# Optimization experiments

Measured on AMD Instinct MI355X. Metric: run time of the kernel, lower is better.

Reference implementation:

```python
import jax, jax.numpy as jnp
import numpy as np

# dims: B batch, R seq_num (MSA rows), L seq_len (residues), D emb_dim, C n_emb_2D, H heads
B, R, L, D, C, H = 1, 256, 384, 512, 256, 4
HD = D // H
SCALE = np.float32((HD ** -0.5) / np.sqrt(L))  # head-dim scaling * seqlen_scaling (1/sqrt(L))
EPS = 1e-5


def setup_inputs() -> dict:
    key = jax.random.key(0)
    ks = jax.random.split(key, 6)
    s = 0.02
    return {
        "x": jax.random.normal(ks[0], (B, R, L, D), jnp.float32),
        "pair_feat": jax.random.normal(ks[1], (B, L, L, C), jnp.float32),
        "attn_mask": jnp.ones((B, L), jnp.int32),
        "ln_msa_g": jnp.ones((D,), jnp.float32),
        "ln_msa_b": jnp.zeros((D,), jnp.float32),
        "ln_pair_g": jnp.ones((C,), jnp.float32),
        "ln_pair_b": jnp.zeros((C,), jnp.float32),
        "W_pair": jax.random.normal(ks[2], (C, H), jnp.float32) * s,  # stacked per-head [C,1] linears
        "W_v": jax.random.normal(ks[3], (D, D), jnp.float32) * s,     # stacked per-head [D,HD] value proj
        "W_out": jax.random.normal(ks[4], (D, D), jnp.float32) * s,   # to_out (bias=False)
    }


def _ln(x, g, b):
    mu = jnp.mean(x, axis=-1, keepdims=True)
    var = jnp.mean(jnp.square(x - mu), axis=-1, keepdims=True)
    return (x - mu) * jax.lax.rsqrt(var + EPS) * g + b


def reference(x, pair_feat, attn_mask, ln_msa_g, ln_msa_b, ln_pair_g, ln_pair_b, W_pair, W_v, W_out):
    # MHPair_to_MSA.forward (eval mode, dropout=0)
    msa = _ln(x, ln_msa_g, ln_msa_b)                                  # [B,R,L,D]
    pf = (pair_feat + jnp.swapaxes(pair_feat, 1, 2)) * 0.5            # symmetrize
    pf = _ln(pf, ln_pair_g, ln_pair_b)                                # [B,L,L,C]
    # pair-feature-derived attention logits (no QK^T)
    logits = jnp.einsum('bijc,ch->bhij', pf * SCALE, W_pair)          # [B,H,L,L]
    V = jnp.einsum('brld,de->brle', msa, W_v).reshape(B, R, L, H, HD) # [B,R,L,H,HD]
    mask2 = attn_mask[:, :, None] * attn_mask[:, None, :]             # [B,L,L]
    logits = jnp.where(mask2[:, None, :, :] == 0,
                       jnp.finfo(logits.dtype).min, logits)
    attn = jax.nn.softmax(logits, axis=-1)                            # [B,H,L,L]
    out = jnp.einsum('bhij,brjhd->brihd', attn, V).reshape(B, R, L, D)
    out = out @ W_out                                                 # to_out, bias=False
    return x + out                                                    # residual
```

## Files before the change

### kernel.cpp

```cpp
#include <hip/hip_runtime.h>

#define L_   384
#define D_   512
#define C_   256
#define H_   4
#define RR_  256
#define M1_  98304
#define LL2_ 147456
#define NPAIR_BLOCKS 18480

typedef __bf16 bf16x8 __attribute__((ext_vector_type(8)));
typedef float f32x4 __attribute__((ext_vector_type(4)));

__device__ __forceinline__ unsigned short f2bf_bits(float f) {
  union { float f; unsigned u; } v; v.f = f;
  return (unsigned short)((v.u + 0x7fffu + ((v.u >> 16) & 1u)) >> 16);
}
__device__ __forceinline__ __bf16 f2bf(float f) {
  union { unsigned short s; __bf16 b; } o; o.s = f2bf_bits(f);
  return o.b;
}

__global__ __launch_bounds__(256) void ln_msa_kernel(
    const float* __restrict__ x, const float* __restrict__ g,
    const float* __restrict__ b, __bf16* __restrict__ msa) {
  int row = blockIdx.x * 4 + (threadIdx.x >> 6);
  int lane = threadIdx.x & 63;
  const float4* xr = (const float4*)(x + (size_t)row * D_ + lane * 8);
  float4 v0 = xr[0], v1 = xr[1];
  float s1 = v0.x + v0.y + v0.z + v0.w + v1.x + v1.y + v1.z + v1.w;
  float s2 = v0.x * v0.x + v0.y * v0.y + v0.z * v0.z + v0.w * v0.w +
             v1.x * v1.x + v1.y * v1.y + v1.z * v1.z + v1.w * v1.w;
#pragma unroll
  for (int o = 32; o > 0; o >>= 1) {
    s1 += __shfl_xor(s1, o);
    s2 += __shfl_xor(s2, o);
  }
  float mu = s1 * (1.0f / D_);
  float var = s2 * (1.0f / D_) - mu * mu;
  float rs = rsqrtf(var + 1e-5f);
  const float4* gp = (const float4*)(g + lane * 8);
  const float4* bp = (const float4*)(b + lane * 8);
  float4 g0 = gp[0], g1 = gp[1], b0 = bp[0], b1 = bp[1];
  float y[8];
  y[0] = (v0.x - mu) * rs * g0.x + b0.x;
  y[1] = (v0.y - mu) * rs * g0.y + b0.y;
  y[2] = (v0.z - mu) * rs * g0.z + b0.z;
  y[3] = (v0.w - mu) * rs * g0.w + b0.w;
  y[4] = (v1.x - mu) * rs * g1.x + b1.x;
  y[5] = (v1.y - mu) * rs * g1.y + b1.y;
  y[6] = (v1.z - mu) * rs * g1.z + b1.z;
  y[7] = (v1.w - mu) * rs * g1.w + b1.w;
  uint4 pk;
  pk.x = ((unsigned)f2bf_bits(y[1]) << 16) | f2bf_bits(y[0]);
  pk.y = ((unsigned)f2bf_bits(y[3]) << 16) | f2bf_bits(y[2]);
  pk.z = ((unsigned)f2bf_bits(y[5]) << 16) | f2bf_bits(y[4]);
  pk.w = ((unsigned)f2bf_bits(y[7]) << 16) | f2bf_bits(y[6]);
  *(uint4*)(msa + (size_t)row * D_ + lane * 8) = pk;
}

__global__ __launch_bounds__(256) void pair_logits_kernel(
    const float* __restrict__ pf, const int* __restrict__ mask,
    const float* __restrict__ g, const float* __restrict__ b,
    const float* __restrict__ Wp, float* __restrict__ logits) {
  unsigned wid = blockIdx.x * 4 + (threadIdx.x >> 6);
  int lane = threadIdx.x & 63;
  unsigned a = wid / 385u;
  unsigned c = wid - a * 385u;
  int i, j;
  if (c < 384u - a) { i = a; j = a + c; }
  else { i = 383 - a; j = i + (c - (384 - a)); }

  int c0 = lane * 4;
  float4 p1 = *(const float4*)(pf + ((size_t)i * L_ + j) * C_ + c0);
  float4 p2 = *(const float4*)(pf + ((size_t)j * L_ + i) * C_ + c0);
  float4 v;
  v.x = 0.5f * (p1.x + p2.x); v.y = 0.5f * (p1.y + p2.y);
  v.z = 0.5f * (p1.z + p2.z); v.w = 0.5f * (p1.w + p2.w);
  float s1 = v.x + v.y + v.z + v.w;
  float s2 = v.x * v.x + v.y * v.y + v.z * v.z + v.w * v.w;
#pragma unroll
  for (int o = 32; o > 0; o >>= 1) {
    s1 += __shfl_xor(s1, o);
    s2 += __shfl_xor(s2, o);
  }
  float mu = s1 * (1.0f / C_);
  float var = s2 * (1.0f / C_) - mu * mu;
  float rs = rsqrtf(var + 1e-5f);
  float4 gv = *(const float4*)(g + c0);
  float4 bv = *(const float4*)(b + c0);
  float y0 = (v.x - mu) * rs * gv.x + bv.x;
  float y1 = (v.y - mu) * rs * gv.y + bv.y;
  float y2 = (v.z - mu) * rs * gv.z + bv.z;
  float y3 = (v.w - mu) * rs * gv.w + bv.w;
  const float4* wp = (const float4*)Wp;
  float4 w0 = wp[c0], w1 = wp[c0 + 1], w2 = wp[c0 + 2], w3 = wp[c0 + 3];
  float4 t;
  t.x = y0 * w0.x + y1 * w1.x + y2 * w2.x + y3 * w3.x;
  t.y = y0 * w0.y + y1 * w1.y + y2 * w2.y + y3 * w3.y;
  t.z = y0 * w0.z + y1 * w1.z + y2 * w2.z + y3 * w3.z;
  t.w = y0 * w0.w + y1 * w1.w + y2 * w2.w + y3 * w3.w;
#pragma unroll
  for (int o = 32; o > 0; o >>= 1) {
    t.x += __shfl_xor(t.x, o);
    t.y += __shfl_xor(t.y, o);
    t.z += __shfl_xor(t.z, o);
    t.w += __shfl_xor(t.w, o);
  }
  if (lane < 8) {
    int h = lane & 3;
    int ii = (lane < 4) ? i : j;
    int jj = (lane < 4) ? j : i;
    bool ok = (mask[i] != 0) && (mask[j] != 0);
    const float NEG = -3.402823466e38f;
    const float SCALE = (float)(0.08838834764831845 / 19.595917942265423);
    float th = (h == 0) ? t.x : (h == 1) ? t.y : (h == 2) ? t.z : t.w;
    logits[(size_t)h * LL2_ + (size_t)ii * L_ + jj] = ok ? SCALE * th : NEG;
  }
}

__global__ __launch_bounds__(256) void softmax_kernel(
    const float* __restrict__ logits, __bf16* __restrict__ attn) {
  int wave = threadIdx.x >> 6, lane = threadIdx.x & 63;
  int row = blockIdx.x * 4 + wave;
  const float* lr = logits + (size_t)row * L_;
  float v[6];
#pragma unroll
  for (int t = 0; t < 6; ++t) v[t] = lr[lane + t * 64];
  float mx = v[0];
#pragma unroll
  for (int t = 1; t < 6; ++t) mx = fmaxf(mx, v[t]);
#pragma unroll
  for (int o = 32; o > 0; o >>= 1) mx = fmaxf(mx, __shfl_xor(mx, o));
  float s = 0.f;
#pragma unroll
  for (int t = 0; t < 6; ++t) { v[t] = __expf(v[t] - mx); s += v[t]; }
#pragma unroll
  for (int o = 32; o > 0; o >>= 1) s += __shfl_xor(s, o);
  float inv = 1.0f / s;
  __bf16* ar = attn + (size_t)row * L_;
#pragma unroll
  for (int t = 0; t < 6; ++t) ar[lane + t * 64] = f2bf(v[t] * inv);
}

__global__ __launch_bounds__(256) void wtrans_kernel(
    const float* __restrict__ Wv, const float* __restrict__ Wo,
    __bf16* __restrict__ WvT, __bf16* __restrict__ WoT) {
  int id = blockIdx.x * 256 + threadIdx.x;
  int m = id >> 18;
  int e = (id >> 9) & 511, d = id & 511;
  const float* W = m ? Wo : Wv;
  __bf16* T = m ? WoT : WvT;
  T[(size_t)e * 512 + d] = f2bf(W[(size_t)d * 512 + e]);
}

__device__ __forceinline__ void gload16(const void* g, void* l) {
  __builtin_amdgcn_global_load_lds(
      (const __attribute__((address_space(1))) void*)g,
      (__attribute__((address_space(3))) void*)l, 16, 0, 0);
}

__device__ __forceinline__ unsigned xcd_swz_768(unsigned bid) {
  return (bid & 7u) * 96u + (bid >> 3);
}

template <int NT>
__device__ __forceinline__ void stage_part32(__bf16* s, const __bf16* g, size_t ld) {
  int tid = threadIdx.x;
#pragma unroll
  for (int i = 0; i < 2; ++i) {
    int cid = i * NT + tid;
    int row = cid >> 2, c = cid & 3;
    int cs = c ^ ((row >> 1) & 3);
    gload16(g + (size_t)row * ld + cs * 8, (char*)s + cid * 16);
  }
}

__device__ __forceinline__ bf16x8 frag_ld32(const __bf16* s, int row, int fk) {
  int c = (fk >> 3) ^ ((row >> 1) & 3);
  return *(const bf16x8*)((const char*)s + row * 64 + c * 16);
}

__device__ __forceinline__ void mainloop256_2s(
    const __bf16* __restrict__ A, size_t ldA,
    const __bf16* __restrict__ B, size_t ldB,
    int K, __bf16* lds, f32x4 acc[8][4]) {
  int lane = threadIdx.x & 63, wave = threadIdx.x >> 6;
  int wm = (wave >> 2) * 128, wn = (wave & 3) * 64;
  int fr = lane & 15, fk = (lane >> 4) * 8;
  int nt = K >> 5;
  const int SLOT = 512 * 32;
  stage_part32<512>(lds, A, ldA);
  stage_part32<512>(lds + 256 * 32, B, ldB);
  for (int t = 0; t < nt; ++t) {
    const __bf16* As = lds + (t & 1) * SLOT;
    const __bf16* Bs = As + 256 * 32;
    if (t + 1 < nt) {
      __bf16* d = lds + ((t + 1) & 1) * SLOT;
      stage_part32<512>(d, A + (size_t)(t + 1) * 32, ldA);
      stage_part32<512>(d + 256 * 32, B + (size_t)(t + 1) * 32, ldB);
      asm volatile("s_waitcnt vmcnt(4)" ::: "memory");
    } else {
      asm volatile("s_waitcnt vmcnt(0)" ::: "memory");
    }
    __builtin_amdgcn_s_barrier();
    bf16x8 bfv[4];
#pragma unroll
    for (int ni = 0; ni < 4; ++ni) bfv[ni] = frag_ld32(Bs, wn + ni * 16 + fr, fk);
#pragma unroll
    for (int half = 0; half < 2; ++half) {
      bf16x8 af[4];
#pragma unroll
      for (int mi = 0; mi < 4; ++mi)
        af[mi] = frag_ld32(As, wm + half * 64 + mi * 16 + fr, fk);
      __builtin_amdgcn_s_setprio(1);
#pragma unroll
      for (int mi = 0; mi < 4; ++mi)
#pragma unroll
        for (int ni = 0; ni < 4; ++ni)
          acc[half * 4 + mi][ni] = __builtin_amdgcn_mfma_f32_16x16x32_bf16(
              af[mi], bfv[ni], acc[half * 4 + mi][ni], 0, 0, 0);
      __builtin_amdgcn_s_setprio(0);
    }
  }
}

__global__ __launch_bounds__(512) void gemm_vt_kernel(
    const __bf16* __restrict__ WvT, const __bf16* __restrict__ msa,
    __bf16* __restrict__ VT) {
  __shared__ __bf16 lds[2 * 512 * 32];
  unsigned swz = xcd_swz_768(blockIdx.x + 2 * blockIdx.y);
  int m0 = (swz & 1) * 256;
  int n0 = (swz >> 1) * 256;
  f32x4 acc[8][4] = {};
  mainloop256_2s(WvT + (size_t)m0 * D_, D_, msa + (size_t)n0 * D_, D_, D_, lds, acc);
  int lane = threadIdx.x & 63, wave = threadIdx.x >> 6;
  int wm = (wave >> 2) * 128, wn = (wave & 3) * 64;
  int cr = (lane >> 4) * 4, cc = lane & 15;
#pragma unroll
  for (int mi = 0; mi < 8; ++mi)
#pragma unroll
    for (int ni = 0; ni < 4; ++ni)
#pragma unroll
      for (int rr = 0; rr < 4; ++rr) {
        int row = m0 + wm + mi * 16 + cr + rr;
        int col = n0 + wn + ni * 16 + cc;
        VT[(size_t)row * M1_ + col] = f2bf(acc[mi][ni][rr]);
      }
}

__global__ __launch_bounds__(512, 1) void attnout_kernel(
    const __bf16* __restrict__ attn, const __bf16* __restrict__ VT,
    const __bf16* __restrict__ WoT, const float* __restrict__ x,
    float* __restrict__ out) {
  __shared__ char lds[98304];
  char* Pl = lds + 65536;
  unsigned swz = xcd_swz_768(blockIdx.x + 3 * blockIdx.y);
  int it = swz % 3u;
  int r  = swz / 3u;
  int tid = threadIdx.x, lane = tid & 63, wave = tid >> 6;
  int fr = lane & 15, fk = (lane >> 4) * 8;
  int cr = (lane >> 4) * 4, cc = lane & 15;
  int wi = (wave >> 2) * 64;
  int we = (wave & 3) * 32;
  int wf = (wave & 3) * 128;

  f32x4 acc_out[4][8] = {};

  for (int h = 0; h < 4; ++h) {
    const __bf16* A = attn + (size_t)h * LL2_ + (size_t)(it * 128) * L_;
    const __bf16* B = VT + (size_t)(h * 128) * M1_ + (size_t)r * L_;

    f32x4 acc_p[4][2] = {};
    {
      const int SLOT = 16384;
      int row = tid >> 2, c = tid & 3;
      int cs = c ^ ((row >> 1) & 3);
      auto stageA = [&](int t) {
        char* d = lds + (t & 3) * SLOT;
        gload16(A + (size_t)row * L_ + t * 32 + cs * 8, d + tid * 16);
        gload16(B + (size_t)row * M1_ + t * 32 + cs * 8, d + 8192 + tid * 16);
      };
      stageA(0); stageA(1); stageA(2);
      for (int t = 0; t < 12; ++t) {
        int rem = 11 - t;
        if (rem >= 2)      asm volatile("s_waitcnt vmcnt(4)" ::: "memory");
        else if (rem == 1) asm volatile("s_waitcnt vmcnt(2)" ::: "memory");
        else               asm volatile("s_waitcnt vmcnt(0)" ::: "memory");
        __builtin_amdgcn_s_barrier();
        const __bf16* As = (const __bf16*)(lds + (t & 3) * SLOT);
        const __bf16* Bs = (const __bf16*)(lds + (t & 3) * SLOT + 8192);
        if (t + 3 < 12) stageA(t + 3);
        bf16x8 af[4], bf2[2];
#pragma unroll
        for (int mi = 0; mi < 4; ++mi) af[mi] = frag_ld32(As, wi + mi * 16 + fr, fk);
#pragma unroll
        for (int ni = 0; ni < 2; ++ni) bf2[ni] = frag_ld32(Bs, we + ni * 16 + fr, fk);
        __builtin_amdgcn_s_setprio(1);
#pragma unroll
        for (int mi = 0; mi < 4; ++mi)
#pragma unroll
          for (int ni = 0; ni < 2; ++ni)
            acc_p[mi][ni] = __builtin_amdgcn_mfma_f32_16x16x32_bf16(
                af[mi], bf2[ni], acc_p[mi][ni], 0, 0, 0);
        __builtin_amdgcn_s_setprio(0);
      }
    }

#pragma unroll
    for (int mi = 0; mi < 4; ++mi)
#pragma unroll
      for (int ni = 0; ni < 2; ++ni)
#pragma unroll
        for (int rr = 0; rr < 4; ++rr) {
          int il = wi + mi * 16 + cr + rr;
          int el = we + ni * 16 + cc;
          *(__bf16*)(Pl + il * 256 + (((el >> 3) ^ (il & 7)) << 4) + (el & 7) * 2) =
              f2bf(acc_p[mi][ni][rr]);
        }
    __syncthreads();

#pragma unroll
    for (int kk = 0; kk < 4; ++kk) {
      int e0 = kk * 32;
      bf16x8 pa[4];
#pragma unroll
      for (int mi = 0; mi < 4; ++mi) {
        int row = wi + mi * 16 + fr;
        int cch = ((e0 + fk) >> 3) ^ (row & 7);
        pa[mi] = *(const bf16x8*)(Pl + row * 256 + (cch << 4));
      }
      bf16x8 wb[8];
#pragma unroll
      for (int ni = 0; ni < 8; ++ni) {
        int f = wf + ni * 16 + fr;
        wb[ni] = *(const bf16x8*)(WoT + (size_t)f * 512 + h * 128 + e0 + fk);
      }
      __builtin_amdgcn_s_setprio(1);
#pragma unroll
      for (int mi = 0; mi < 4; ++mi)
#pragma unroll
        for (int ni = 0; ni < 8; ++ni)
          acc_out[mi][ni] = __builtin_amdgcn_mfma_f32_16x16x32_bf16(
              pa[mi], wb[ni], acc_out[mi][ni], 0, 0, 0);
      __builtin_amdgcn_s_setprio(0);
    }
    __syncthreads();
  }

  int mrow0 = r * L_ + it * 128 + wi;
#pragma unroll
  for (int mi = 0; mi < 4; ++mi)
#pragma unroll
    for (int ni = 0; ni < 8; ++ni)
#pragma unroll
      for (int rr = 0; rr < 4; ++rr) {
        int row = mrow0 + mi * 16 + cr + rr;
        int col = wf + ni * 16 + cc;
        size_t idx = (size_t)row * D_ + col;
        out[idx] = x[idx] + acc_out[mi][ni][rr];
      }
}

extern "C" void kernel_launch(void* const* d_in, const int* in_sizes, int n_in,
                              void* d_out, int out_size, void* d_ws, size_t ws_size,
                              hipStream_t stream) {
  const float* x      = (const float*)d_in[0];
  const float* pair   = (const float*)d_in[1];
  const int*   mask   = (const int*)d_in[2];
  const float* g_msa  = (const float*)d_in[3];
  const float* b_msa  = (const float*)d_in[4];
  const float* g_pair = (const float*)d_in[5];
  const float* b_pair = (const float*)d_in[6];
  const float* Wp     = (const float*)d_in[7];
  const float* Wv     = (const float*)d_in[8];
  const float* Wo     = (const float*)d_in[9];
  float* out = (float*)d_out;

  char* p = (char*)d_ws;
  auto alloc = [&](size_t bytes) {
    char* r = p;
    p += (bytes + 255) & ~(size_t)255;
    return r;
  };
  __bf16* msa    = (__bf16*)alloc((size_t)M1_ * D_ * 2);
  __bf16* VT     = (__bf16*)alloc((size_t)D_ * M1_ * 2);
  float*  logits = (float*)alloc((size_t)H_ * LL2_ * 4);
  __bf16* attn   = (__bf16*)alloc((size_t)H_ * LL2_ * 2);
  __bf16* WvT    = (__bf16*)alloc((size_t)512 * 512 * 2);
  __bf16* WoT    = (__bf16*)alloc((size_t)512 * 512 * 2);

  wtrans_kernel<<<2048, 256, 0, stream>>>(Wv, Wo, WvT, WoT);
  ln_msa_kernel<<<M1_ / 4, 256, 0, stream>>>(x, g_msa, b_msa, msa);
  gemm_vt_kernel<<<dim3(2, M1_ / 256), 512, 0, stream>>>(WvT, msa, VT);
  pair_logits_kernel<<<NPAIR_BLOCKS, 256, 0, stream>>>(pair, mask, g_pair, b_pair, Wp, logits);
  softmax_kernel<<<(H_ * L_) / 4, 256, 0, stream>>>(logits, attn);
  attnout_kernel<<<dim3(3, RR_), 512, 0, stream>>>(attn, VT, WoT, x, out);
}
```

Measured before the change: 403.2 us.

## Double-buffer attnout staging across heads and pad P tile instead of swizzle

Replaces the per-head 4-slot, 3-deep prefetch pipeline in attnout_kernel with a continuous 2-slot double buffer that prefetches the next tile, including the first tile of the next head, so the pipeline no longer drains and refills at each head boundary. LDS use drops from 96KB to 66KB. The XOR-swizzled P buffer is replaced with a padded row stride of 272 bytes. The aim is to remove per-head pipeline bubbles, but only one tile of prefetch depth hides less global latency, and the padding may change bank-conflict behaviour.

```diff
diff --git a/kernel.cpp b/kernel.cpp
--- a/kernel.cpp
+++ b/kernel.cpp
@@ -253,8 +253,8 @@
     const __bf16* __restrict__ attn, const __bf16* __restrict__ VT,
     const __bf16* __restrict__ WoT, const float* __restrict__ x,
     float* __restrict__ out) {
-  __shared__ char lds[98304];
-  char* Pl = lds + 65536;
+  __shared__ char lds[67584];
+  char* Pl = lds + 32768;
   unsigned swz = xcd_swz_768(blockIdx.x + 3 * blockIdx.y);
   int it = swz % 3u;
   int r  = swz / 3u;
@@ -265,46 +265,46 @@
   int we = (wave & 3) * 32;
   int wf = (wave & 3) * 128;
 
+  const __bf16* A0 = attn + (size_t)(it * 128) * L_;
+  const __bf16* B0 = VT + (size_t)r * L_;
+
+  int srow = tid >> 2;
+  int scs = (tid & 3) ^ ((srow >> 1) & 3);
+  auto stageA = [&](int h, int t, int s) {
+    char* d = lds + s * 16384;
+    gload16(A0 + (size_t)h * LL2_ + (size_t)srow * L_ + t * 32 + scs * 8,
+            d + tid * 16);
+    gload16(B0 + (size_t)(h * 128 + srow) * M1_ + t * 32 + scs * 8,
+            d + 8192 + tid * 16);
+  };
+
   f32x4 acc_out[4][8] = {};
 
+  stageA(0, 0, 0);
   for (int h = 0; h < 4; ++h) {
-    const __bf16* A = attn + (size_t)h * LL2_ + (size_t)(it * 128) * L_;
-    const __bf16* B = VT + (size_t)(h * 128) * M1_ + (size_t)r * L_;
-
     f32x4 acc_p[4][2] = {};
-    {
-      const int SLOT = 16384;
-      int row = tid >> 2, c = tid & 3;
-      int cs = c ^ ((row >> 1) & 3);
-      auto stageA = [&](int t) {
-        char* d = lds + (t & 3) * SLOT;
-        gload16(A + (size_t)row * L_ + t * 32 + cs * 8, d + tid * 16);
-        gload16(B + (size_t)row * M1_ + t * 32 + cs * 8, d + 8192 + tid * 16);
-      };
-      stageA(0); stageA(1); stageA(2);
-      for (int t = 0; t < 12; ++t) {
-        int rem = 11 - t;
-        if (rem >= 2)      asm volatile("s_waitcnt vmcnt(4)" ::: "memory");
-        else if (rem == 1) asm volatile("s_waitcnt vmcnt(2)" ::: "memory");
-        else               asm volatile("s_waitcnt vmcnt(0)" ::: "memory");
-        __builtin_amdgcn_s_barrier();
-        const __bf16* As = (const __bf16*)(lds + (t & 3) * SLOT);
-        const __bf16* Bs = (const __bf16*)(lds + (t & 3) * SLOT + 8192);
-        if (t + 3 < 12) stageA(t + 3);
-        bf16x8 af[4], bf2[2];
-#pragma unroll
-        for (int mi = 0; mi < 4; ++mi) af[mi] = frag_ld32(As, wi + mi * 16 + fr, fk);
-#pragma unroll
-        for (int ni = 0; ni < 2; ++ni) bf2[ni] = frag_ld32(Bs, we + ni * 16 + fr, fk);
-        __builtin_amdgcn_s_setprio(1);
-#pragma unroll
-        for (int mi = 0; mi < 4; ++mi)
-#pragma unroll
-          for (int ni = 0; ni < 2; ++ni)
-            acc_p[mi][ni] = __builtin_amdgcn_mfma_f32_16x16x32_bf16(
-                af[mi], bf2[ni], acc_p[mi][ni], 0, 0, 0);
-        __builtin_amdgcn_s_setprio(0);
-      }
+    for (int t = 0; t < 12; ++t) {
+      int ft = h * 12 + t;
+      if (t + 1 < 12)      stageA(h, t + 1, (ft + 1) & 1);
+      else if (h + 1 < 4)  stageA(h + 1, 0, (ft + 1) & 1);
+      if (ft == 47) asm volatile("s_waitcnt vmcnt(0)" ::: "memory");
+      else          asm volatile("s_waitcnt vmcnt(2)" ::: "memory");
+      __builtin_amdgcn_s_barrier();
+      const __bf16* As = (const __bf16*)(lds + (ft & 1) * 16384);
+      const __bf16* Bs = (const __bf16*)(lds + (ft & 1) * 16384 + 8192);
+      bf16x8 af[4], bf2[2];
+#pragma unroll
+      for (int mi = 0; mi < 4; ++mi) af[mi] = frag_ld32(As, wi + mi * 16 + fr, fk);
+#pragma unroll
+      for (int ni = 0; ni < 2; ++ni) bf2[ni] = frag_ld32(Bs, we + ni * 16 + fr, fk);
+      __builtin_amdgcn_s_setprio(1);
+#pragma unroll
+      for (int mi = 0; mi < 4; ++mi)
+#pragma unroll
+        for (int ni = 0; ni < 2; ++ni)
+          acc_p[mi][ni] = __builtin_amdgcn_mfma_f32_16x16x32_bf16(
+              af[mi], bf2[ni], acc_p[mi][ni], 0, 0, 0);
+      __builtin_amdgcn_s_setprio(0);
     }
 
 #pragma unroll
@@ -315,8 +315,7 @@
         for (int rr = 0; rr < 4; ++rr) {
           int il = wi + mi * 16 + cr + rr;
           int el = we + ni * 16 + cc;
-          *(__bf16*)(Pl + il * 256 + (((el >> 3) ^ (il & 7)) << 4) + (el & 7) * 2) =
-              f2bf(acc_p[mi][ni][rr]);
+          *(__bf16*)(Pl + il * 272 + el * 2) = f2bf(acc_p[mi][ni][rr]);
         }
     __syncthreads();
 
@@ -325,17 +324,13 @@
       int e0 = kk * 32;
       bf16x8 pa[4];
 #pragma unroll
-      for (int mi = 0; mi < 4; ++mi) {
-        int row = wi + mi * 16 + fr;
-        int cch = ((e0 + fk) >> 3) ^ (row & 7);
-        pa[mi] = *(const bf16x8*)(Pl + row * 256 + (cch << 4));
-      }
+      for (int mi = 0; mi < 4; ++mi)
+        pa[mi] = *(const bf16x8*)(Pl + (wi + mi * 16 + fr) * 272 + (e0 + fk) * 2);
       bf16x8 wb[8];
 #pragma unroll
-      for (int ni = 0; ni < 8; ++ni) {
-        int f = wf + ni * 16 + fr;
-        wb[ni] = *(const bf16x8*)(WoT + (size_t)f * 512 + h * 128 + e0 + fk);
-      }
+      for (int ni = 0; ni < 8; ++ni)
+        wb[ni] = *(const bf16x8*)(WoT + (size_t)(wf + ni * 16 + fr) * 512 +
+                                  h * 128 + e0 + fk);
       __builtin_amdgcn_s_setprio(1);
 #pragma unroll
       for (int mi = 0; mi < 4; ++mi)
```

Result: no change. 401.6 us (-0.4%).
